# Performance work log

Hardware: AMD Instinct MI355X
Metric: run time of the kernel (lower is better)

Reference implementation:

```python
import jax, jax.numpy as jnp
import numpy as np
import math

NM = 1024
NH = 16
ND = NM // NH
B, L = 4, 1024


def setup_inputs() -> dict:
    key = jax.random.key(0)
    ks = jax.random.split(key, 11)
    s = 1.0 / math.sqrt(NM)
    return {
        "x": jax.random.normal(ks[0], (B, L, NM), dtype=jnp.float32),
        "mask": jax.random.randint(ks[1], (B, L, L), 0, 2, dtype=jnp.int32),
        "Wq": jax.random.normal(ks[2], (NM, NM), dtype=jnp.float32) * s,
        "bq": jax.random.normal(ks[3], (NM,), dtype=jnp.float32) * 0.01,
        "Wk": jax.random.normal(ks[4], (NM, NM), dtype=jnp.float32) * s,
        "bk": jax.random.normal(ks[5], (NM,), dtype=jnp.float32) * 0.01,
        "Wv": jax.random.normal(ks[6], (NM, NM), dtype=jnp.float32) * s,
        "bv": jax.random.normal(ks[7], (NM,), dtype=jnp.float32) * 0.01,
        "Wo": jax.random.normal(ks[8], (NM, NM), dtype=jnp.float32) * s,
        "bo": jax.random.normal(ks[9], (NM,), dtype=jnp.float32) * 0.01,
    }


def reference(x, mask, Wq, bq, Wk, bk, Wv, bv, Wo, bo):
    nB, nL, _ = x.shape
    m = mask.astype(x.dtype)  # [B,L,L]
    # QKV projections (torch Linear: y = x @ W.T + b)
    q = (x @ Wq.T + bq).reshape(nB, nL, NH, ND)
    k = (x @ Wk.T + bk).reshape(nB, nL, NH, ND)
    v = (x @ Wv.T + bv).reshape(nB, nL, NH, ND)
    # scaled dot product; NOTE: module scales by 1/sqrt(nM), not 1/sqrt(nD)
    scores = jnp.einsum("bqhd,bkhd->bhqk", q, k) / math.sqrt(NM)
    # additive/multiplicative padding mask: S*mask - (1-mask)*1e9
    mb = m[:, None, :, :]  # broadcast over heads [B,1,L,L]
    scores = scores * mb - (1.0 - mb) * 1e9
    attn = jax.nn.softmax(scores, axis=-1)
    ctx = jnp.einsum("bhqk,bkhd->bqhd", attn, v).reshape(nB, nL, NM)
    out = ctx @ Wo.T + bo
    return out
```

## Files before the change

kernel.cpp:

```cpp
#include <hip/hip_runtime.h>

typedef unsigned short u16;
typedef unsigned int   u32;
typedef unsigned long long u64;
typedef __attribute__((ext_vector_type(8))) short    short8;
typedef __attribute__((ext_vector_type(4))) float    floatx4;
typedef __attribute__((ext_vector_type(4))) _Float16 half4v;
typedef __attribute__((ext_vector_type(8))) _Float16 half8v;

#define NM 1024
#define NH 16
#define ND 64
#define BB 4
#define LL 1024
#define MM (BB*LL)

__device__ __forceinline__ u16 f2bf(float f) {
  union { float f; u32 u; } c; c.f = f;
  u32 u = c.u;
  return (u16)((u + 0x7fffu + ((u >> 16) & 1u)) >> 16);
}

__device__ __forceinline__ void cstore(u16* p, float v)  { *p = f2bf(v); }
__device__ __forceinline__ void cstore(float* p, float v){ *p = v; }

__device__ __forceinline__ void load_lds16(const void* g, void* l) {
  __builtin_amdgcn_global_load_lds((const __attribute__((address_space(1))) u32*)g,
                                   (__attribute__((address_space(3))) u32*)l,
                                   16, 0, 0);
}

__device__ __forceinline__ int vperm(int K) {
  return (K & ~31) | (((K >> 2) & 3) << 3) | (((K >> 4) & 1) << 2) | (K & 3);
}

__global__ void conv_all(const float* __restrict__ x,  const float* __restrict__ Wq,
                         const float* __restrict__ Wk, const float* __restrict__ Wv,
                         const float* __restrict__ Wo,
                         u16* __restrict__ xb, u16* __restrict__ wcat, u16* __restrict__ wob) {
  const int y = blockIdx.y;
  const float* src; u16* dst;
  if      (y == 0) { src = x;  dst = xb; }
  else if (y == 1) { src = Wq; dst = wcat; }
  else if (y == 2) { src = Wk; dst = wcat + NM * NM; }
  else if (y == 3) { src = Wv; dst = wcat + 2 * NM * NM; }
  else             { src = Wo; dst = wob; }
  const int nrep = (y == 0) ? 4 : 1;
  const int base = blockIdx.x * 256 + threadIdx.x;
  for (int t = 0; t < nrep; t++) {
    int i = (base + t * 262144) * 4;
    float4 v = *(const float4*)(src + i);
    ushort4 o;
    o.x = f2bf(v.x); o.y = f2bf(v.y); o.z = f2bf(v.z); o.w = f2bf(v.w);
    *(ushort4*)(dst + i) = o;
  }
}

__global__ void pack_mask(const int* __restrict__ m, u32* __restrict__ mp) {
  int i = blockIdx.x * blockDim.x + threadIdx.x;
  int v = m[i];
  u64 b = __ballot(v != 0);
  int lane = threadIdx.x & 63;
  if (lane == 0) {
    mp[(i >> 5) + 0] = (u32)b;
    mp[(i >> 5) + 1] = (u32)(b >> 32);
  }
}

template<int TM, int TN, typename OUT_T, bool TRANS_Z2>
__global__ __launch_bounds__(256)
void gemm_bt_kernel(const u16* __restrict__ A,
                    const u16* __restrict__ Ball,
                    const float* __restrict__ b0, const float* __restrict__ b1,
                    const float* __restrict__ b2,
                    OUT_T* __restrict__ Call,
                    _Float16* __restrict__ VTout)
{
  constexpr int K = 1024, N = 1024;
  constexpr int NI = TM / 32, NJ = TN / 32;
  constexpr int CH = (TM + TN) / 16;
  const int z = blockIdx.z;
  const u16* Bm = Ball + (size_t)z * N * K;
  const float* bias = (z == 0) ? b0 : ((z == 1) ? b1 : b2);
  OUT_T* C = Call + (size_t)z * MM * N;

  __shared__ u16 S[(TM + TN) * 32];
  u16* As = S;
  u16* Bs = S + TM * 32;

  const int tid = threadIdx.x;
  const int w = tid >> 6, lane = tid & 63, lane15 = lane & 15, quad = lane >> 4;
  const int row0 = blockIdx.x * TM, col0 = blockIdx.y * TN;
  const int wm = (w >> 1) * (TM / 2), wn = (w & 1) * (TN / 2);
  const int sr = lane >> 2, sc = (lane & 3) * 8;

  floatx4 acc[NI][NJ];
  const floatx4 zero = {0.f, 0.f, 0.f, 0.f};
  #pragma unroll
  for (int i = 0; i < NI; i++)
    #pragma unroll
    for (int j = 0; j < NJ; j++) acc[i][j] = zero;

  for (int kk = 0; kk < K; kk += 32) {
    __syncthreads();
    #pragma unroll
    for (int c = 0; c < CH / 4; c++) {
      int g = w * (CH / 4) + c;
      const u16* src;
      if (g * 16 < TM) src = A  + (size_t)(row0 + g * 16 + sr) * K + kk + sc;
      else             src = Bm + (size_t)(col0 + (g * 16 - TM) + sr) * K + kk + sc;
      load_lds16(src, &S[g * 512]);
    }
    __syncthreads();

    short8 af[NI], bf[NJ];
    #pragma unroll
    for (int i = 0; i < NI; i++)
      af[i] = *(short8*)&As[(wm + i * 16 + lane15) * 32 + quad * 8];
    #pragma unroll
    for (int j = 0; j < NJ; j++)
      bf[j] = *(short8*)&Bs[(wn + j * 16 + lane15) * 32 + quad * 8];
    #pragma unroll
    for (int i = 0; i < NI; i++)
      #pragma unroll
      for (int j = 0; j < NJ; j++)
        acc[i][j] = __builtin_amdgcn_mfma_f32_16x16x32_bf16(af[i], bf[j], acc[i][j], 0, 0, 0);
  }

  #pragma unroll
  for (int i = 0; i < NI; i++) {
    #pragma unroll
    for (int j = 0; j < NJ; j++) {
      int col = col0 + wn + j * 16 + lane15;
      float bv = bias[col];
      if (TRANS_Z2 && z == 2) {
        int row = row0 + wm + i * 16 + quad * 4;
        int Kk = row & (LL - 1), bb = row & ~(LL - 1);
        int o = vperm(Kk);
        half4v hv;
        hv.x = (_Float16)(acc[i][j][0] + bv);
        hv.y = (_Float16)(acc[i][j][1] + bv);
        hv.z = (_Float16)(acc[i][j][2] + bv);
        hv.w = (_Float16)(acc[i][j][3] + bv);
        *(half4v*)&VTout[(size_t)col * MM + bb + o] = hv;
      } else {
        #pragma unroll
        for (int r = 0; r < 4; r++) {
          int row = row0 + wm + i * 16 + quad * 4 + r;
          cstore(&C[(size_t)row * N + col], acc[i][j][r] + bv);
        }
      }
    }
  }
}

__global__ __launch_bounds__(256, 4)
void attn_kernel(const u16* __restrict__ Q, const u16* __restrict__ K,
                 const _Float16* __restrict__ VT, const u32* __restrict__ mp,
                 u16* __restrict__ CTX)
{
  __shared__ u16      Ks[2 * 128 * 32];
  __shared__ _Float16 Vs[64 * 128];

  const int tid = threadIdx.x;
  const int w = tid >> 6, lane = tid & 63, lane15 = lane & 15, quad = lane >> 4;
  const int qt = blockIdx.x, bh = blockIdx.y;
  const int b = bh >> 4, h = bh & 15;
  const int q0 = qt * 64 + w * 16;
  const size_t kvbase = (size_t)(b * LL) * NM + h * ND;
  const size_t vtbase = (size_t)(h * ND) * MM + (size_t)b * LL;
  const float scale = 0.03125f;

  short8 aq[2];
  {
    const u16* qp = Q + (size_t)(b * LL + q0 + lane15) * NM + h * ND + quad * 8;
    aq[0] = *(const short8*)(qp);
    aq[1] = *(const short8*)(qp + 32);
  }

  const int ksrow = lane >> 2;
  const int kscg  = (lane & 3) ^ (ksrow & 3);
  const int vsd   = lane >> 4;
  const int vscg  = (lane & 15);

  const floatx4 zero = {0.f, 0.f, 0.f, 0.f};
  floatx4 o_acc[4] = {zero, zero, zero, zero};
  float lsum = 0.f;

  const u32* mrow = mp + (size_t)(b * LL + q0 + lane15) * 32;

  #pragma unroll 1
  for (int kt = 0; kt < 8; kt++) {
    const int k0 = kt * 128;
    const uint4 m4 = *(const uint4*)(mrow + kt * 4);

    __syncthreads();
    #pragma unroll
    for (int t = 0; t < 4; t++) {
      int n = w * 4 + t;
      int s = n & 1, r0 = (n >> 1) * 16;
      int row = r0 + ksrow;
      load_lds16(K + kvbase + (size_t)(k0 + row) * NM + s * 32 + kscg * 8,
                 &Ks[n * 512]);
    }
    #pragma unroll
    for (int t = 0; t < 4; t++) {
      int n = w * 4 + t;
      int d = n * 4 + vsd;
      int cg = vscg ^ (d & 15);
      load_lds16(VT + vtbase + (size_t)d * MM + k0 + cg * 8, &Vs[n * 512]);
    }
    __syncthreads();

    half4v pf[8];
    #pragma unroll
    for (int j = 0; j < 8; j++) {
      const int ch = (quad ^ (lane15 & 3)) * 8;
      const int kbase = j * 1024 + lane15 * 32 + ch;
      const short8 kf0 = *(const short8*)&Ks[kbase];
      const short8 kf1 = *(const short8*)&Ks[kbase + 512];
      floatx4 sT = zero;
      sT = __builtin_amdgcn_mfma_f32_16x16x32_bf16(kf0, aq[0], sT, 0, 0, 0);
      sT = __builtin_amdgcn_mfma_f32_16x16x32_bf16(kf1, aq[1], sT, 0, 0, 0);
      const u32 mw = (j & 2) ? ((j & 4) ? m4.w : m4.y) : ((j & 4) ? m4.z : m4.x);
      const int sh = (j & 1) * 16 + quad * 4;
      float p[4];
      #pragma unroll
      for (int r = 0; r < 4; r++) {
        float e = __expf(sT[r] * scale);
        p[r] = ((mw >> (sh + r)) & 1u) ? e : 0.f;
        lsum += p[r];
      }
      const auto lo = __builtin_amdgcn_cvt_pkrtz(p[0], p[1]);
      const auto hi = __builtin_amdgcn_cvt_pkrtz(p[2], p[3]);
      half4v pj;
      pj.x = (_Float16)lo.x; pj.y = (_Float16)lo.y;
      pj.z = (_Float16)hi.x; pj.w = (_Float16)hi.y;
      pf[j] = pj;
    }

    #pragma unroll
    for (int jd = 0; jd < 4; jd++) {
      const int d = jd * 16 + lane15;
      #pragma unroll
      for (int j2 = 0; j2 < 4; j2++) {
        const int cidx = (j2 * 4 + quad) ^ (d & 15);
        const half8v vv = *(const half8v*)&Vs[d * 128 + cidx * 8];
        const half4v vlo = __builtin_shufflevector(vv, vv, 0, 1, 2, 3);
        const half4v vhi = __builtin_shufflevector(vv, vv, 4, 5, 6, 7);
        o_acc[jd] = __builtin_amdgcn_mfma_f32_16x16x16f16(vlo, pf[2 * j2],     o_acc[jd], 0, 0, 0);
        o_acc[jd] = __builtin_amdgcn_mfma_f32_16x16x16f16(vhi, pf[2 * j2 + 1], o_acc[jd], 0, 0, 0);
      }
    }
  }

  lsum += __shfl_xor(lsum, 16);
  lsum += __shfl_xor(lsum, 32);
  const float inv = 1.0f / lsum;

  const size_t obase = (size_t)(b * LL + q0 + lane15) * NM + h * ND;
  #pragma unroll
  for (int jd = 0; jd < 4; jd++) {
    ushort4 o;
    o.x = f2bf(o_acc[jd][0] * inv);
    o.y = f2bf(o_acc[jd][1] * inv);
    o.z = f2bf(o_acc[jd][2] * inv);
    o.w = f2bf(o_acc[jd][3] * inv);
    *(ushort4*)(CTX + obase + jd * 16 + quad * 4) = o;
  }
}

extern "C" void kernel_launch(void* const* d_in, const int* in_sizes, int n_in,
                              void* d_out, int out_size, void* d_ws, size_t ws_size,
                              hipStream_t stream) {
  const float* x  = (const float*)d_in[0];
  const int*   mk = (const int*)  d_in[1];
  const float* Wq = (const float*)d_in[2]; const float* bq = (const float*)d_in[3];
  const float* Wk = (const float*)d_in[4]; const float* bk = (const float*)d_in[5];
  const float* Wv = (const float*)d_in[6]; const float* bv = (const float*)d_in[7];
  const float* Wo = (const float*)d_in[8]; const float* bo = (const float*)d_in[9];
  float* out = (float*)d_out;

  char* ws = (char*)d_ws;
  u16* xb        = (u16*)(ws);
  u16* Wcat      = (u16*)(ws + ((size_t)8  << 20));
  u16* Wob       = (u16*)(ws + ((size_t)14 << 20));
  u16* QKb       = (u16*)(ws + ((size_t)16 << 20));
  _Float16* VT   = (_Float16*)(ws + ((size_t)32 << 20));
  u16* CTX       = (u16*)(ws + ((size_t)40 << 20));
  u32* mp        = (u32*)(ws + ((size_t)48 << 20));

  conv_all<<<dim3(1024, 5), 256, 0, stream>>>(x, Wq, Wk, Wv, Wo, xb, Wcat, Wob);
  pack_mask<<<16384, 256, 0, stream>>>(mk, mp);

  gemm_bt_kernel<128, 128, u16, true><<<dim3(32, 8, 3), 256, 0, stream>>>(
      xb, Wcat, bq, bk, bv, QKb, VT);

  attn_kernel<<<dim3(16, 64), 256, 0, stream>>>(
      QKb, QKb + (size_t)MM * NM, VT, mp, CTX);

  gemm_bt_kernel<64, 128, float, false><<<dim3(64, 8, 1), 256, 0, stream>>>(
      CTX, Wob, bo, bo, bo, out, nullptr);
}
```

Measured before the change: 203.5 us.

## Process two query tiles per attention block and fuse mask packing into conversion kernel

After: 198.1 us. 2.6% less time.

```diff
diff --git a/kernel.cpp b/kernel.cpp
--- a/kernel.cpp
+++ b/kernel.cpp
@@ -36,9 +36,25 @@
 
 __global__ void conv_all(const float* __restrict__ x,  const float* __restrict__ Wq,
                          const float* __restrict__ Wk, const float* __restrict__ Wv,
-                         const float* __restrict__ Wo,
-                         u16* __restrict__ xb, u16* __restrict__ wcat, u16* __restrict__ wob) {
+                         const float* __restrict__ Wo, const int* __restrict__ m,
+                         u16* __restrict__ xb, u16* __restrict__ wcat,
+                         u16* __restrict__ wob, u32* __restrict__ mp) {
   const int y = blockIdx.y;
+  const int base = blockIdx.x * 256 + threadIdx.x;
+  if (y == 5) {
+    const int lane = threadIdx.x & 63;
+    #pragma unroll
+    for (int t = 0; t < 16; t++) {
+      int i = base + t * 262144;
+      int v = m[i];
+      u64 bits = __ballot(v != 0);
+      if (lane == 0) {
+        mp[(i >> 5) + 0] = (u32)bits;
+        mp[(i >> 5) + 1] = (u32)(bits >> 32);
+      }
+    }
+    return;
+  }
   const float* src; u16* dst;
   if      (y == 0) { src = x;  dst = xb; }
   else if (y == 1) { src = Wq; dst = wcat; }
@@ -46,24 +62,12 @@
   else if (y == 3) { src = Wv; dst = wcat + 2 * NM * NM; }
   else             { src = Wo; dst = wob; }
   const int nrep = (y == 0) ? 4 : 1;
-  const int base = blockIdx.x * 256 + threadIdx.x;
   for (int t = 0; t < nrep; t++) {
     int i = (base + t * 262144) * 4;
     float4 v = *(const float4*)(src + i);
     ushort4 o;
     o.x = f2bf(v.x); o.y = f2bf(v.y); o.z = f2bf(v.z); o.w = f2bf(v.w);
     *(ushort4*)(dst + i) = o;
-  }
-}
-
-__global__ void pack_mask(const int* __restrict__ m, u32* __restrict__ mp) {
-  int i = blockIdx.x * blockDim.x + threadIdx.x;
-  int v = m[i];
-  u64 b = __ballot(v != 0);
-  int lane = threadIdx.x & 63;
-  if (lane == 0) {
-    mp[(i >> 5) + 0] = (u32)b;
-    mp[(i >> 5) + 1] = (u32)(b >> 32);
   }
 }
 
@@ -154,7 +158,7 @@
   }
 }
 
-__global__ __launch_bounds__(256, 4)
+__global__ __launch_bounds__(256, 2)
 void attn_kernel(const u16* __restrict__ Q, const u16* __restrict__ K,
                  const _Float16* __restrict__ VT, const u32* __restrict__ mp,
                  u16* __restrict__ CTX)
@@ -164,18 +168,22 @@
 
   const int tid = threadIdx.x;
   const int w = tid >> 6, lane = tid & 63, lane15 = lane & 15, quad = lane >> 4;
-  const int qt = blockIdx.x, bh = blockIdx.y;
+  const int qb = blockIdx.x * 128, bh = blockIdx.y;
   const int b = bh >> 4, h = bh & 15;
-  const int q0 = qt * 64 + w * 16;
   const size_t kvbase = (size_t)(b * LL) * NM + h * ND;
   const size_t vtbase = (size_t)(h * ND) * MM + (size_t)b * LL;
   const float scale = 0.03125f;
 
-  short8 aq[2];
-  {
-    const u16* qp = Q + (size_t)(b * LL + q0 + lane15) * NM + h * ND + quad * 8;
-    aq[0] = *(const short8*)(qp);
-    aq[1] = *(const short8*)(qp + 32);
+  int q0g[2];
+  q0g[0] = qb + w * 16;
+  q0g[1] = qb + 64 + w * 16;
+
+  short8 aq[2][2];
+  #pragma unroll
+  for (int g = 0; g < 2; g++) {
+    const u16* qp = Q + (size_t)(b * LL + q0g[g] + lane15) * NM + h * ND + quad * 8;
+    aq[g][0] = *(const short8*)(qp);
+    aq[g][1] = *(const short8*)(qp + 32);
   }
 
   const int ksrow = lane >> 2;
@@ -184,15 +192,15 @@
   const int vscg  = (lane & 15);
 
   const floatx4 zero = {0.f, 0.f, 0.f, 0.f};
-  floatx4 o_acc[4] = {zero, zero, zero, zero};
-  float lsum = 0.f;
-
-  const u32* mrow = mp + (size_t)(b * LL + q0 + lane15) * 32;
+  floatx4 o_acc[2][4] = {{zero, zero, zero, zero}, {zero, zero, zero, zero}};
+  float lsum[2] = {0.f, 0.f};
+
+  const u32* mrow0 = mp + (size_t)(b * LL + q0g[0] + lane15) * 32;
+  const u32* mrow1 = mp + (size_t)(b * LL + q0g[1] + lane15) * 32;
 
   #pragma unroll 1
   for (int kt = 0; kt < 8; kt++) {
     const int k0 = kt * 128;
-    const uint4 m4 = *(const uint4*)(mrow + kt * 4);
 
     __syncthreads();
     #pragma unroll
@@ -212,61 +220,70 @@
     }
     __syncthreads();
 
-    half4v pf[8];
-    #pragma unroll
-    for (int j = 0; j < 8; j++) {
-      const int ch = (quad ^ (lane15 & 3)) * 8;
-      const int kbase = j * 1024 + lane15 * 32 + ch;
-      const short8 kf0 = *(const short8*)&Ks[kbase];
-      const short8 kf1 = *(const short8*)&Ks[kbase + 512];
-      floatx4 sT = zero;
-      sT = __builtin_amdgcn_mfma_f32_16x16x32_bf16(kf0, aq[0], sT, 0, 0, 0);
-      sT = __builtin_amdgcn_mfma_f32_16x16x32_bf16(kf1, aq[1], sT, 0, 0, 0);
-      const u32 mw = (j & 2) ? ((j & 4) ? m4.w : m4.y) : ((j & 4) ? m4.z : m4.x);
-      const int sh = (j & 1) * 16 + quad * 4;
-      float p[4];
+    #pragma unroll
+    for (int g = 0; g < 2; g++) {
+      const u32* mrow = g ? mrow1 : mrow0;
+      const uint4 m4 = *(const uint4*)(mrow + kt * 4);
+
+      half4v pf[8];
       #pragma unroll
-      for (int r = 0; r < 4; r++) {
-        float e = __expf(sT[r] * scale);
-        p[r] = ((mw >> (sh + r)) & 1u) ? e : 0.f;
-        lsum += p[r];
+      for (int j = 0; j < 8; j++) {
+        const int ch = (quad ^ (lane15 & 3)) * 8;
+        const int kbase = j * 1024 + lane15 * 32 + ch;
+        const short8 kf0 = *(const short8*)&Ks[kbase];
+        const short8 kf1 = *(const short8*)&Ks[kbase + 512];
+        floatx4 sT = zero;
+        sT = __builtin_amdgcn_mfma_f32_16x16x32_bf16(kf0, aq[g][0], sT, 0, 0, 0);
+        sT = __builtin_amdgcn_mfma_f32_16x16x32_bf16(kf1, aq[g][1], sT, 0, 0, 0);
+        const u32 mw = (j & 2) ? ((j & 4) ? m4.w : m4.y) : ((j & 4) ? m4.z : m4.x);
+        const int sh = (j & 1) * 16 + quad * 4;
+        float p[4];
+        #pragma unroll
+        for (int r = 0; r < 4; r++) {
+          float e = __expf(sT[r] * scale);
+          p[r] = ((mw >> (sh + r)) & 1u) ? e : 0.f;
+          lsum[g] += p[r];
+        }
+        const auto lo = __builtin_amdgcn_cvt_pkrtz(p[0], p[1]);
+        const auto hi = __builtin_amdgcn_cvt_pkrtz(p[2], p[3]);
+        half4v pj;
+        pj.x = (_Float16)lo.x; pj.y = (_Float16)lo.y;
+        pj.z = (_Float16)hi.x; pj.w = (_Float16)hi.y;
+        pf[j] = pj;
       }
-      const auto lo = __builtin_amdgcn_cvt_pkrtz(p[0], p[1]);
-      const auto hi = __builtin_amdgcn_cvt_pkrtz(p[2], p[3]);
-      half4v pj;
-      pj.x = (_Float16)lo.x; pj.y = (_Float16)lo.y;
-      pj.z = (_Float16)hi.x; pj.w = (_Float16)hi.y;
-      pf[j] = pj;
-    }
-
+
+      #pragma unroll
+      for (int jd = 0; jd < 4; jd++) {
+        const int d = jd * 16 + lane15;
+        #pragma unroll
+        for (int j2 = 0; j2 < 4; j2++) {
+          const int cidx = (j2 * 4 + quad) ^ (d & 15);
+          const half8v vv = *(const half8v*)&Vs[d * 128 + cidx * 8];
+          const half4v vlo = __builtin_shufflevector(vv, vv, 0, 1, 2, 3);
+          const half4v vhi = __builtin_shufflevector(vv, vv, 4, 5, 6, 7);
+          o_acc[g][jd] = __builtin_amdgcn_mfma_f32_16x16x16f16(vlo, pf[2 * j2],     o_acc[g][jd], 0, 0, 0);
+          o_acc[g][jd] = __builtin_amdgcn_mfma_f32_16x16x16f16(vhi, pf[2 * j2 + 1], o_acc[g][jd], 0, 0, 0);
+        }
+      }
+    }
+  }
+
+  #pragma unroll
+  for (int g = 0; g < 2; g++) {
+    float ls = lsum[g];
+    ls += __shfl_xor(ls, 16);
+    ls += __shfl_xor(ls, 32);
+    const float inv = 1.0f / ls;
+    const size_t obase = (size_t)(b * LL + q0g[g] + lane15) * NM + h * ND;
     #pragma unroll
     for (int jd = 0; jd < 4; jd++) {
-      const int d = jd * 16 + lane15;
-      #pragma unroll
-      for (int j2 = 0; j2 < 4; j2++) {
-        const int cidx = (j2 * 4 + quad) ^ (d & 15);
-        const half8v vv = *(const half8v*)&Vs[d * 128 + cidx * 8];
-        const half4v vlo = __builtin_shufflevector(vv, vv, 0, 1, 2, 3);
-        const half4v vhi = __builtin_shufflevector(vv, vv, 4, 5, 6, 7);
-        o_acc[jd] = __builtin_amdgcn_mfma_f32_16x16x16f16(vlo, pf[2 * j2],     o_acc[jd], 0, 0, 0);
-        o_acc[jd] = __builtin_amdgcn_mfma_f32_16x16x16f16(vhi, pf[2 * j2 + 1], o_acc[jd], 0, 0, 0);
-      }
-    }
-  }
-
-  lsum += __shfl_xor(lsum, 16);
-  lsum += __shfl_xor(lsum, 32);
-  const float inv = 1.0f / lsum;
-
-  const size_t obase = (size_t)(b * LL + q0 + lane15) * NM + h * ND;
-  #pragma unroll
-  for (int jd = 0; jd < 4; jd++) {
-    ushort4 o;
-    o.x = f2bf(o_acc[jd][0] * inv);
-    o.y = f2bf(o_acc[jd][1] * inv);
-    o.z = f2bf(o_acc[jd][2] * inv);
-    o.w = f2bf(o_acc[jd][3] * inv);
-    *(ushort4*)(CTX + obase + jd * 16 + quad * 4) = o;
+      ushort4 o;
+      o.x = f2bf(o_acc[g][jd][0] * inv);
+      o.y = f2bf(o_acc[g][jd][1] * inv);
+      o.z = f2bf(o_acc[g][jd][2] * inv);
+      o.w = f2bf(o_acc[g][jd][3] * inv);
+      *(ushort4*)(CTX + obase + jd * 16 + quad * 4) = o;
+    }
   }
 }
 
@@ -290,13 +307,13 @@
   u16* CTX       = (u16*)(ws + ((size_t)40 << 20));
   u32* mp        = (u32*)(ws + ((size_t)48 << 20));
 
-  conv_all<<<dim3(1024, 5), 256, 0, stream>>>(x, Wq, Wk, Wv, Wo, xb, Wcat, Wob);
-  pack_mask<<<16384, 256, 0, stream>>>(mk, mp);
+  conv_all<<<dim3(1024, 6), 256, 0, stream>>>(x, Wq, Wk, Wv, Wo, mk,
+                                              xb, Wcat, Wob, mp);
 
   gemm_bt_kernel<128, 128, u16, true><<<dim3(32, 8, 3), 256, 0, stream>>>(
       xb, Wcat, bq, bk, bv, QKb, VT);
 
-  attn_kernel<<<dim3(16, 64), 256, 0, stream>>>(
+  attn_kernel<<<dim3(8, 64), 256, 0, stream>>>(
       QKb, QKb + (size_t)MM * NM, VT, mp, CTX);
 
   gemm_bt_kernel<64, 128, float, false><<<dim3(64, 8, 1), 256, 0, stream>>>(
```
